# Performance work log

Measured on AMD Instinct MI355X. Metric: run time of the kernel, lower is better.

Reference implementation:

```python
import jax, jax.numpy as jnp
import numpy as np

C = 256
NUM_HEADS = 8
HEAD_DIM = C // NUM_HEADS
SCALE = HEAD_DIM ** -0.5


def setup_inputs() -> dict:
    key = jax.random.key(0)
    ks = jax.random.split(key, 10)
    B, H, W = 2, 64, 64
    s = 0.02
    return {
        "spatial_feat": jax.random.normal(ks[0], (B, C, H, W), jnp.float32),
        "freq_feat": jax.random.normal(ks[1], (B, C, H, W), jnp.float32),
        "wq": jax.random.normal(ks[2], (C, C), jnp.float32) * s,
        "bq": jax.random.normal(ks[3], (C,), jnp.float32) * s,
        "wk": jax.random.normal(ks[4], (C, C), jnp.float32) * s,
        "bk": jax.random.normal(ks[5], (C,), jnp.float32) * s,
        "wv": jax.random.normal(ks[6], (C, C), jnp.float32) * s,
        "bv": jax.random.normal(ks[7], (C,), jnp.float32) * s,
        "wo": jax.random.normal(ks[8], (C, C), jnp.float32) * s,
        "bo": jax.random.normal(ks[9], (C,), jnp.float32) * s,
    }


def _proj(x, w, b):
    # 1x1 conv == channel-mixing matmul: (O,C) x (B,C,H,W) -> (B,O,H,W)
    return jnp.einsum('oc,bchw->bohw', w, x) + b[None, :, None, None]


def _heads(x, B, HW):
    return x.reshape(B, NUM_HEADS, HEAD_DIM, HW)


def _cross_attend(q_src, kv_src, wq, bq, wk, bk, wv, bv, wo, bo):
    B, Cc, H, W = q_src.shape
    HW = H * W
    q = _heads(_proj(q_src, wq, bq), B, HW)   # (B, h, d, N)
    k = _heads(_proj(kv_src, wk, bk), B, HW)
    v = _heads(_proj(kv_src, wv, bv), B, HW)
    # attn[b,h,m,n] = q[...,m] . k[...,n]
    attn = jnp.einsum('bhdm,bhdn->bhmn', q, k) * SCALE
    attn = jax.nn.softmax(attn, axis=-1)
    # out[...,m] = sum_n v[...,n] * attn[m,n]
    out = jnp.einsum('bhdn,bhmn->bhdm', v, attn)
    out = out.reshape(B, Cc, H, W)
    return _proj(out, wo, bo)


def reference(spatial_feat, freq_feat, wq, bq, wk, bk, wv, bv, wo, bo):
    spatial_attended = spatial_feat + _cross_attend(
        spatial_feat, freq_feat, wq, bq, wk, bk, wv, bv, wo, bo)
    freq_attended = freq_feat + _cross_attend(
        freq_feat, spatial_feat, wq, bq, wk, bk, wv, bv, wo, bo)
    return spatial_attended + freq_attended
```

## Files before the change

kernel.cpp:

```cpp
#include <hip/hip_runtime.h>
#include <hip/hip_bf16.h>

#define B_ 2
#define C_ 256
#define NH_ 8
#define D_ 32
#define N_ 4096
#define SCALE_ 0.17677669529663689f
#define QSC_ 0.25505277f

typedef __hip_bfloat16 bf16;
typedef __attribute__((ext_vector_type(8))) short sx8;
typedef __attribute__((ext_vector_type(4))) short sx4;
typedef __attribute__((ext_vector_type(4))) float fx4;
typedef __attribute__((ext_vector_type(4))) int ix4;

__device__ __forceinline__ float b2f(bf16 x) { return __bfloat162float(x); }
__device__ __forceinline__ bf16 f2b(float x) { return __float2bfloat16(x); }
__device__ __forceinline__ short fbs(float x) { bf16 h = __float2bfloat16(x); return *(short*)&h; }
__device__ __forceinline__ float sbf(short s) { bf16 h = *(bf16*)&s; return __bfloat162float(h); }

#if __has_builtin(__builtin_amdgcn_exp2f)
__device__ __forceinline__ float fexp2(float x) { return __builtin_amdgcn_exp2f(x); }
#else
__device__ __forceinline__ float fexp2(float x) { return exp2f(x); }
#endif

__device__ __forceinline__ unsigned pkbf_tr(float x, float y) {
#if __has_builtin(__builtin_amdgcn_perm)
  return __builtin_amdgcn_perm(__builtin_bit_cast(unsigned, y),
                               __builtin_bit_cast(unsigned, x), 0x07060302u);
#else
  unsigned a = __builtin_bit_cast(unsigned, x) >> 16;
  unsigned b = __builtin_bit_cast(unsigned, y) & 0xFFFF0000u;
  return a | b;
#endif
}
__device__ __forceinline__ void pl32swap(unsigned &a, unsigned &b) {
  asm volatile("v_permlane32_swap_b32 %0, %1" : "+v"(a), "+v"(b));
}
__device__ __forceinline__ void pl16swap(unsigned &a, unsigned &b) {
  asm volatile("v_permlane16_swap_b32 %0, %1" : "+v"(a), "+v"(b));
}

__global__ __launch_bounds__(256)
void convert_kernel(const float* __restrict__ spatial,
                    const float* __restrict__ freq,
                    const float* __restrict__ wq, const float* __restrict__ wk,
                    const float* __restrict__ wv, const float* __restrict__ wo,
                    bf16* __restrict__ xb, bf16* __restrict__ wb,
                    bf16* __restrict__ wob) {
  const int tid = threadIdx.x;
  if (blockIdx.z == 4) {
    int base = (blockIdx.y * 64 + blockIdx.x) * 256 + tid;
    #pragma unroll
    for (int i = 0; i < 4; ++i) {
      int idx = base + i * 65536;
      if (idx < 196608) {
        const float* src = (idx < 65536) ? wq : (idx < 131072) ? wk : wv;
        wb[idx] = f2b(src[idx & 65535]);
      } else {
        wob[idx - 196608] = f2b(wo[idx - 196608]);
      }
    }
    return;
  }

  const int p0 = blockIdx.x * 64;
  const int c0 = blockIdx.y * 64;
  const int z  = blockIdx.z;
  const int s = z >> 1, b = z & 1;
  const float* x = (s == 0) ? spatial : freq;

  __shared__ float ls[64][65];

  const int pp = tid & 63, cb = tid >> 6;
  #pragma unroll
  for (int i = 0; i < 16; ++i) {
    int c = cb + 4 * i;
    ls[c][pp] = x[(size_t)(b * C_ + c0 + c) * N_ + p0 + pp];
  }
  __syncthreads();

  #pragma unroll
  for (int i = 0; i < 2; ++i) {
    int j = tid + 256 * i;
    int p = j >> 3, ck = (j & 7) * 8;
    short tmp[8];
    #pragma unroll
    for (int u = 0; u < 8; ++u) tmp[u] = fbs(ls[ck + u][p]);
    *(sx8*)(xb + ((size_t)z * N_ + p0 + p) * C_ + c0 + ck) = *(sx8*)tmp;
  }
}

__global__ __launch_bounds__(256)
void qkv_gemm_kernel(const bf16* __restrict__ wb, const bf16* __restrict__ xb,
                     const float* __restrict__ bq, const float* __restrict__ bk,
                     const float* __restrict__ bv,
                     bf16* __restrict__ qhf, bf16* __restrict__ khf,
                     bf16* __restrict__ vhf) {
  const int tid = threadIdx.x;
  const int p0 = blockIdx.x * 128;
  const int o0 = blockIdx.y * 128;
  const int z  = blockIdx.z;

  const int lane = tid & 63, w = tid >> 6;
  const int ml = lane & 15, Q4 = (lane >> 4) * 4, Q8 = (lane >> 4) * 8;
  const int ow = (w >> 1) * 64, pw = (w & 1) * 64;

  __shared__ __align__(16) short asb[128 * 72];
  __shared__ __align__(16) short bsb[128 * 72];
  __shared__ float bias_s[128];

  if (tid < 128) {
    int o = o0 + tid;
    bias_s[tid] = (o < 256) ? bq[o] : (o < 512) ? bk[o - 256] : bv[o - 512];
  }

  const fx4 z4 = {0.f, 0.f, 0.f, 0.f};
  fx4 acc[4][4];
  #pragma unroll
  for (int ot = 0; ot < 4; ++ot)
    #pragma unroll
    for (int pt = 0; pt < 4; ++pt) acc[ot][pt] = z4;

  const int sr = tid >> 1, scu = (tid & 1) * 32;
  for (int k0 = 0; k0 < 256; k0 += 64) {
    __syncthreads();
    #pragma unroll
    for (int u = 0; u < 4; ++u) {
      *(sx8*)&asb[sr * 72 + scu + u * 8] =
          *(const sx8*)&wb[(o0 + sr) * 256 + k0 + scu + u * 8];
      *(sx8*)&bsb[sr * 72 + scu + u * 8] =
          *(const sx8*)(xb + ((size_t)z * N_ + p0 + sr) * C_ + k0 + scu + u * 8);
    }
    __syncthreads();
    #pragma unroll
    for (int kk = 0; kk < 2; ++kk) {
      sx8 af[4], bfr[4];
      #pragma unroll
      for (int t = 0; t < 4; ++t)
        af[t] = *(sx8*)&asb[(ow + t * 16 + ml) * 72 + kk * 32 + Q8];
      #pragma unroll
      for (int t = 0; t < 4; ++t)
        bfr[t] = *(sx8*)&bsb[(pw + t * 16 + ml) * 72 + kk * 32 + Q8];
      #pragma unroll
      for (int ot = 0; ot < 4; ++ot)
        #pragma unroll
        for (int pt = 0; pt < 4; ++pt)
          acc[ot][pt] = __builtin_amdgcn_mfma_f32_16x16x32_bf16(
              af[ot], bfr[pt], acc[ot][pt], 0, 0, 0);
    }
  }

  if (o0 < 512) {
    bf16* dst = (o0 < 256) ? qhf : khf;
    const int ob = (o0 < 256) ? o0 : o0 - 256;
    const float scl = (o0 < 256) ? QSC_ : 1.f;
    #pragma unroll
    for (int ot = 0; ot < 4; ++ot) {
      const int og = ob + ow + ot * 16 + Q4;
      #pragma unroll
      for (int pt = 0; pt < 4; ++pt) {
        int p = p0 + pw + pt * 16 + ml;
        short tmp[4];
        #pragma unroll
        for (int r = 0; r < 4; ++r)
          tmp[r] = fbs((acc[ot][pt][r] + bias_s[ow + ot * 16 + Q4 + r]) * scl);
        *(sx4*)(dst + (((size_t)z * NH_ + (og >> 5)) * N_ + p) * D_ + (og & 31)) =
            *(sx4*)tmp;
      }
    }
  } else {
    #pragma unroll
    for (int ot = 0; ot < 4; ++ot)
      #pragma unroll
      for (int pt = 0; pt < 4; ++pt) {
        int p = p0 + pw + pt * 16 + ml;
        #pragma unroll
        for (int r = 0; r < 4; ++r) {
          int lo = ow + ot * 16 + Q4 + r;
          int rho = (o0 - 512) + lo;
          int h = rho >> 5, d = rho & 31;
          size_t basev = ((size_t)z * NH_ + h) * D_ * N_;
          vhf[basev + (size_t)(((p >> 5) * 2) + (d >> 4)) * 512 +
              (d & 15) * 32 + (p & 31)] = f2b(acc[ot][pt][r] + bias_s[lo]);
        }
      }
  }
}

__global__ __launch_bounds__(256, 2)
void attn_kernel(const bf16* __restrict__ qhf, const bf16* __restrict__ khf,
                 const bf16* __restrict__ vhf, bf16* __restrict__ attoT) {
  const int tid  = threadIdx.x;
  const int m0   = blockIdx.x * 256;
  const int h    = blockIdx.y;
  const int z    = blockIdx.z;
  const int s = z >> 1, b = z & 1;
  const int zo = ((1 - s) << 1) | b;

  const bf16* qz = qhf + ((size_t)z  * NH_ + h) * N_ * D_;
  const bf16* kz = khf + ((size_t)zo * NH_ + h) * N_ * D_;
  const bf16* vz = vhf + ((size_t)zo * NH_ + h) * D_ * N_;

  const int lane = tid & 63;
  const int w    = tid >> 6;
  const int ml   = lane & 15;
  const int q4   = lane >> 4;
  const int Q4   = q4 * 4;
  const int Q8   = q4 * 8;

  __shared__ __align__(16) short kts[2][64 * 32];
  __shared__ __align__(16) short vss[2][4][16 * 36];

  sx8 qf[4];
  #pragma unroll
  for (int s4 = 0; s4 < 4; ++s4)
    qf[s4] = *(const sx8*)(qz + (size_t)(m0 + w * 64 + s4 * 16 + ml) * D_ + Q8);

  sx8 onesf;
  #pragma unroll
  for (int u = 0; u < 8; ++u) onesf[u] = (short)0x3F80;

  const fx4 z4 = {0.f, 0.f, 0.f, 0.f};
  fx4 acc[4][2];
  #pragma unroll
  for (int s4 = 0; s4 < 4; ++s4) { acc[s4][0] = z4; acc[s4][1] = z4; }
  fx4 lacc[4] = {z4, z4, z4, z4};

  const int srow = tid >> 2;
  const int ksw  = ((tid & 3) ^ (srow & 3)) * 8;
  const int vblk = tid >> 6, vrow = (tid >> 2) & 15, vg = (tid & 3) * 8;
  const int kfg  = (q4 ^ (ml & 3)) * 8;

  sx8 kpre = *(const sx8*)(kz + (size_t)tid * 8);
  sx8 vpre = *(const sx8*)(vz + (size_t)tid * 8);
  *(sx8*)&kts[0][srow * 32 + ksw] = kpre;
  *(sx8*)&vss[0][vblk][vrow * 36 + vg] = vpre;
  __syncthreads();

  int cur = 0;
  for (int n0 = 0; n0 < N_; n0 += 64) {
    const bool more = (n0 + 64 < N_);
    if (more) {
      kpre = *(const sx8*)(kz + (size_t)(n0 + 64) * D_ + (size_t)tid * 8);
      vpre = *(const sx8*)(vz + (size_t)(n0 + 64) * D_ + (size_t)tid * 8);
    }

    sx8 kf[4], vf[2][2];
    #pragma unroll
    for (int t = 0; t < 4; ++t)
      kf[t] = *(sx8*)&kts[cur][(t * 16 + ml) * 32 + kfg];
    #pragma unroll
    for (int dt = 0; dt < 2; ++dt)
      #pragma unroll
      for (int c = 0; c < 2; ++c)
        vf[dt][c] = *(sx8*)&vss[cur][c * 2 + dt][ml * 36 + Q8];

    #pragma unroll
    for (int s4 = 0; s4 < 4; ++s4) {
      fx4 st[4];
      #pragma unroll
      for (int t = 0; t < 4; ++t)
        st[t] = __builtin_amdgcn_mfma_f32_16x16x32_bf16(kf[t], qf[s4], z4, 0, 0, 0);

      unsigned T[4][2];
      #pragma unroll
      for (int t = 0; t < 4; ++t) {
        float e0 = fexp2(st[t][0]), e1 = fexp2(st[t][1]);
        float e2 = fexp2(st[t][2]), e3 = fexp2(st[t][3]);
        T[t][0] = pkbf_tr(e0, e1);
        T[t][1] = pkbf_tr(e2, e3);
      }
      pl32swap(T[0][0], T[1][0]); pl16swap(T[0][0], T[1][0]);
      pl32swap(T[0][1], T[1][1]); pl16swap(T[0][1], T[1][1]);
      pl32swap(T[2][0], T[3][0]); pl16swap(T[2][0], T[3][0]);
      pl32swap(T[2][1], T[3][1]); pl16swap(T[2][1], T[3][1]);
      ix4 p0 = {(int)T[0][0], (int)T[0][1], (int)T[1][0], (int)T[1][1]};
      ix4 p1 = {(int)T[2][0], (int)T[2][1], (int)T[3][0], (int)T[3][1]};
      sx8 pf0 = *(sx8*)&p0;
      sx8 pf1 = *(sx8*)&p1;

      lacc[s4] = __builtin_amdgcn_mfma_f32_16x16x32_bf16(onesf, pf0, lacc[s4], 0, 0, 0);
      lacc[s4] = __builtin_amdgcn_mfma_f32_16x16x32_bf16(onesf, pf1, lacc[s4], 0, 0, 0);
      #pragma unroll
      for (int dt = 0; dt < 2; ++dt) {
        fx4 a = acc[s4][dt];
        a = __builtin_amdgcn_mfma_f32_16x16x32_bf16(vf[dt][0], pf0, a, 0, 0, 0);
        a = __builtin_amdgcn_mfma_f32_16x16x32_bf16(vf[dt][1], pf1, a, 0, 0, 0);
        acc[s4][dt] = a;
      }
    }

    if (more) {
      *(sx8*)&kts[cur ^ 1][srow * 32 + ksw] = kpre;
      *(sx8*)&vss[cur ^ 1][vblk][vrow * 36 + vg] = vpre;
    }
    __syncthreads();
    cur ^= 1;
  }

  #pragma unroll
  for (int s4 = 0; s4 < 4; ++s4) {
    float inv = 1.f / lacc[s4][0];
    int col = m0 + w * 64 + s4 * 16 + ml;
    #pragma unroll
    for (int dt = 0; dt < 2; ++dt) {
      short tmp[4];
      #pragma unroll
      for (int r = 0; r < 4; ++r) tmp[r] = fbs(acc[s4][dt][r] * inv);
      *(sx4*)(attoT + ((size_t)z * N_ + col) * C_ + h * D_ + dt * 16 + Q4) =
          *(sx4*)tmp;
    }
  }
}

__global__ __launch_bounds__(256)
void out_proj_kernel(const bf16* __restrict__ wob, const bf16* __restrict__ attoT,
                     const float* __restrict__ spatial,
                     const float* __restrict__ freq,
                     const float* __restrict__ bo, float* __restrict__ out) {
  const int tid = threadIdx.x;
  const int p0 = blockIdx.x * 64;
  const int o0 = blockIdx.y * 64;
  const int b  = blockIdx.z;

  const int lane = tid & 63, w = tid >> 6;
  const int ml = lane & 15, Q4 = (lane >> 4) * 4, Q8 = (lane >> 4) * 8;
  const int ow = (w >> 1) * 32, pw = (w & 1) * 32;

  __shared__ __align__(16) short asb[64 * 72];
  __shared__ __align__(16) short bsb[64 * 72];
  __shared__ float bo_s[64];

  if (tid < 64) bo_s[tid] = 2.f * bo[o0 + tid];

  const bf16* at0 = attoT + (size_t)(0 + b) * N_ * C_;
  const bf16* at1 = attoT + (size_t)(2 + b) * N_ * C_;

  const fx4 z4 = {0.f, 0.f, 0.f, 0.f};
  fx4 acc[2][2];
  #pragma unroll
  for (int ot = 0; ot < 2; ++ot)
    #pragma unroll
    for (int pt = 0; pt < 2; ++pt) acc[ot][pt] = z4;

  for (int k0 = 0; k0 < 256; k0 += 64) {
    __syncthreads();
    #pragma unroll
    for (int i = 0; i < 2; ++i) {
      int j = tid + 256 * i;
      int r = j >> 3, cu = (j & 7) * 8;
      *(sx8*)&asb[r * 72 + cu] = *(const sx8*)&wob[(o0 + r) * 256 + k0 + cu];
      sx8 va = *(const sx8*)(at0 + (size_t)(p0 + r) * C_ + k0 + cu);
      sx8 vb2 = *(const sx8*)(at1 + (size_t)(p0 + r) * C_ + k0 + cu);
      short tmp[8];
      #pragma unroll
      for (int u = 0; u < 8; ++u) tmp[u] = fbs(sbf(va[u]) + sbf(vb2[u]));
      *(sx8*)&bsb[r * 72 + cu] = *(sx8*)tmp;
    }
    __syncthreads();
    #pragma unroll
    for (int kk = 0; kk < 2; ++kk) {
      sx8 af[2], bfr[2];
      #pragma unroll
      for (int t = 0; t < 2; ++t)
        af[t] = *(sx8*)&asb[(ow + t * 16 + ml) * 72 + kk * 32 + Q8];
      #pragma unroll
      for (int t = 0; t < 2; ++t)
        bfr[t] = *(sx8*)&bsb[(pw + t * 16 + ml) * 72 + kk * 32 + Q8];
      #pragma unroll
      for (int ot = 0; ot < 2; ++ot)
        #pragma unroll
        for (int pt = 0; pt < 2; ++pt)
          acc[ot][pt] = __builtin_amdgcn_mfma_f32_16x16x32_bf16(
              af[ot], bfr[pt], acc[ot][pt], 0, 0, 0);
    }
  }

  #pragma unroll
  for (int ot = 0; ot < 2; ++ot)
    #pragma unroll
    for (int pt = 0; pt < 2; ++pt) {
      int p = p0 + pw + pt * 16 + ml;
      #pragma unroll
      for (int r = 0; r < 4; ++r) {
        int ol = ow + ot * 16 + Q4 + r;
        size_t off = ((size_t)b * C_ + o0 + ol) * N_ + p;
        out[off] = acc[ot][pt][r] + bo_s[ol] + spatial[off] + freq[off];
      }
    }
}

extern "C" void kernel_launch(void* const* d_in, const int* in_sizes, int n_in,
                              void* d_out, int out_size, void* d_ws, size_t ws_size,
                              hipStream_t stream) {
  const float* spatial = (const float*)d_in[0];
  const float* freq    = (const float*)d_in[1];
  const float* wq = (const float*)d_in[2];
  const float* bq = (const float*)d_in[3];
  const float* wk = (const float*)d_in[4];
  const float* bk = (const float*)d_in[5];
  const float* wv = (const float*)d_in[6];
  const float* bv = (const float*)d_in[7];
  const float* wo = (const float*)d_in[8];
  const float* bo = (const float*)d_in[9];
  float* out = (float*)d_out;

  const size_t SZ = (size_t)2 * B_ * N_ * C_;
  bf16* xb    = (bf16*)d_ws;
  bf16* qhf   = xb + SZ;
  bf16* khf   = qhf + SZ;
  bf16* vhf   = khf + SZ;
  bf16* attoT = vhf + SZ;
  bf16* wb    = attoT + SZ;
  bf16* wob   = wb + 768 * 256;

  convert_kernel<<<dim3(N_ / 64, C_ / 64, 5), 256, 0, stream>>>(
      spatial, freq, wq, wk, wv, wo, xb, wb, wob);
  qkv_gemm_kernel<<<dim3(N_ / 128, 768 / 128, 2 * B_), 256, 0, stream>>>(
      wb, xb, bq, bk, bv, qhf, khf, vhf);
  attn_kernel<<<dim3(N_ / 256, NH_, 2 * B_), 256, 0, stream>>>(
      qhf, khf, vhf, attoT);
  out_proj_kernel<<<dim3(N_ / 64, C_ / 64, B_), 256, 0, stream>>>(
      wob, attoT, spatial, freq, bo, out);
}
```

Before: 203.7 us.

## Load K/V fragments directly from global into registers, drop LDS staging

The attention loop no longer stages K and V tiles through double-buffered shared memory with a barrier per tile. Each lane now loads its MFMA fragments straight from global memory into two register sets, prefetching the next tile while computing the current one, and the block-wide syncs are gone. s_setprio is also raised around the MFMA bursts. The aim is to remove LDS traffic and barrier stalls, at the cost of more global/L2 loads, because every wave now fetches the same K/V data, and higher register pressure. On the last iteration the prefetch wraps to tile 0 and loads data that is never used.

```diff
diff --git a/kernel.cpp b/kernel.cpp
--- a/kernel.cpp
+++ b/kernel.cpp
@@ -190,6 +190,50 @@
   }
 }
 
+__device__ __forceinline__ void attn_tile(const sx8 kf[4], const sx8 vf[2][2],
+                                          const sx8 qf[4], sx8 onesf,
+                                          fx4 acc[4][2], fx4 lacc[4]) {
+  const fx4 z4 = {0.f, 0.f, 0.f, 0.f};
+  #pragma unroll
+  for (int s4 = 0; s4 < 4; ++s4) {
+    fx4 st[4];
+    __builtin_amdgcn_s_setprio(1);
+    #pragma unroll
+    for (int t = 0; t < 4; ++t)
+      st[t] = __builtin_amdgcn_mfma_f32_16x16x32_bf16(kf[t], qf[s4], z4, 0, 0, 0);
+    __builtin_amdgcn_s_setprio(0);
+
+    unsigned T[4][2];
+    #pragma unroll
+    for (int t = 0; t < 4; ++t) {
+      float e0 = fexp2(st[t][0]), e1 = fexp2(st[t][1]);
+      float e2 = fexp2(st[t][2]), e3 = fexp2(st[t][3]);
+      T[t][0] = pkbf_tr(e0, e1);
+      T[t][1] = pkbf_tr(e2, e3);
+    }
+    pl32swap(T[0][0], T[1][0]); pl16swap(T[0][0], T[1][0]);
+    pl32swap(T[0][1], T[1][1]); pl16swap(T[0][1], T[1][1]);
+    pl32swap(T[2][0], T[3][0]); pl16swap(T[2][0], T[3][0]);
+    pl32swap(T[2][1], T[3][1]); pl16swap(T[2][1], T[3][1]);
+    ix4 p0 = {(int)T[0][0], (int)T[0][1], (int)T[1][0], (int)T[1][1]};
+    ix4 p1 = {(int)T[2][0], (int)T[2][1], (int)T[3][0], (int)T[3][1]};
+    sx8 pf0 = *(sx8*)&p0;
+    sx8 pf1 = *(sx8*)&p1;
+
+    __builtin_amdgcn_s_setprio(1);
+    lacc[s4] = __builtin_amdgcn_mfma_f32_16x16x32_bf16(onesf, pf0, lacc[s4], 0, 0, 0);
+    lacc[s4] = __builtin_amdgcn_mfma_f32_16x16x32_bf16(onesf, pf1, lacc[s4], 0, 0, 0);
+    #pragma unroll
+    for (int dt = 0; dt < 2; ++dt) {
+      fx4 a = acc[s4][dt];
+      a = __builtin_amdgcn_mfma_f32_16x16x32_bf16(vf[dt][0], pf0, a, 0, 0, 0);
+      a = __builtin_amdgcn_mfma_f32_16x16x32_bf16(vf[dt][1], pf1, a, 0, 0, 0);
+      acc[s4][dt] = a;
+    }
+    __builtin_amdgcn_s_setprio(0);
+  }
+}
+
 __global__ __launch_bounds__(256, 2)
 void attn_kernel(const bf16* __restrict__ qhf, const bf16* __restrict__ khf,
                  const bf16* __restrict__ vhf, bf16* __restrict__ attoT) {
@@ -211,9 +255,6 @@
   const int Q4   = q4 * 4;
   const int Q8   = q4 * 8;
 
-  __shared__ __align__(16) short kts[2][64 * 32];
-  __shared__ __align__(16) short vss[2][4][16 * 36];
-
   sx8 qf[4];
   #pragma unroll
   for (int s4 = 0; s4 < 4; ++s4)
@@ -229,77 +270,40 @@
   for (int s4 = 0; s4 < 4; ++s4) { acc[s4][0] = z4; acc[s4][1] = z4; }
   fx4 lacc[4] = {z4, z4, z4, z4};
 
-  const int srow = tid >> 2;
-  const int ksw  = ((tid & 3) ^ (srow & 3)) * 8;
-  const int vblk = tid >> 6, vrow = (tid >> 2) & 15, vg = (tid & 3) * 8;
-  const int kfg  = (q4 ^ (ml & 3)) * 8;
-
-  sx8 kpre = *(const sx8*)(kz + (size_t)tid * 8);
-  sx8 vpre = *(const sx8*)(vz + (size_t)tid * 8);
-  *(sx8*)&kts[0][srow * 32 + ksw] = kpre;
-  *(sx8*)&vss[0][vblk][vrow * 36 + vg] = vpre;
-  __syncthreads();
-
-  int cur = 0;
-  for (int n0 = 0; n0 < N_; n0 += 64) {
-    const bool more = (n0 + 64 < N_);
-    if (more) {
-      kpre = *(const sx8*)(kz + (size_t)(n0 + 64) * D_ + (size_t)tid * 8);
-      vpre = *(const sx8*)(vz + (size_t)(n0 + 64) * D_ + (size_t)tid * 8);
-    }
-
-    sx8 kf[4], vf[2][2];
-    #pragma unroll
-    for (int t = 0; t < 4; ++t)
-      kf[t] = *(sx8*)&kts[cur][(t * 16 + ml) * 32 + kfg];
-    #pragma unroll
-    for (int dt = 0; dt < 2; ++dt)
-      #pragma unroll
-      for (int c = 0; c < 2; ++c)
-        vf[dt][c] = *(sx8*)&vss[cur][c * 2 + dt][ml * 36 + Q8];
-
-    #pragma unroll
-    for (int s4 = 0; s4 < 4; ++s4) {
-      fx4 st[4];
-      #pragma unroll
-      for (int t = 0; t < 4; ++t)
-        st[t] = __builtin_amdgcn_mfma_f32_16x16x32_bf16(kf[t], qf[s4], z4, 0, 0, 0);
-
-      unsigned T[4][2];
-      #pragma unroll
-      for (int t = 0; t < 4; ++t) {
-        float e0 = fexp2(st[t][0]), e1 = fexp2(st[t][1]);
-        float e2 = fexp2(st[t][2]), e3 = fexp2(st[t][3]);
-        T[t][0] = pkbf_tr(e0, e1);
-        T[t][1] = pkbf_tr(e2, e3);
-      }
-      pl32swap(T[0][0], T[1][0]); pl16swap(T[0][0], T[1][0]);
-      pl32swap(T[0][1], T[1][1]); pl16swap(T[0][1], T[1][1]);
-      pl32swap(T[2][0], T[3][0]); pl16swap(T[2][0], T[3][0]);
-      pl32swap(T[2][1], T[3][1]); pl16swap(T[2][1], T[3][1]);
-      ix4 p0 = {(int)T[0][0], (int)T[0][1], (int)T[1][0], (int)T[1][1]};
-      ix4 p1 = {(int)T[2][0], (int)T[2][1], (int)T[3][0], (int)T[3][1]};
-      sx8 pf0 = *(sx8*)&p0;
-      sx8 pf1 = *(sx8*)&p1;
-
-      lacc[s4] = __builtin_amdgcn_mfma_f32_16x16x32_bf16(onesf, pf0, lacc[s4], 0, 0, 0);
-      lacc[s4] = __builtin_amdgcn_mfma_f32_16x16x32_bf16(onesf, pf1, lacc[s4], 0, 0, 0);
-      #pragma unroll
-      for (int dt = 0; dt < 2; ++dt) {
-        fx4 a = acc[s4][dt];
-        a = __builtin_amdgcn_mfma_f32_16x16x32_bf16(vf[dt][0], pf0, a, 0, 0, 0);
-        a = __builtin_amdgcn_mfma_f32_16x16x32_bf16(vf[dt][1], pf1, a, 0, 0, 0);
-        acc[s4][dt] = a;
-      }
-    }
-
-    if (more) {
-      *(sx8*)&kts[cur ^ 1][srow * 32 + ksw] = kpre;
-      *(sx8*)&vss[cur ^ 1][vblk][vrow * 36 + vg] = vpre;
-    }
-    __syncthreads();
-    cur ^= 1;
-  }
+  const bf16* kbase = kz + (size_t)ml * D_ + Q8;
+  const bf16* vbase = vz + (size_t)ml * 32 + Q8;
+
+#define LDK(n0, kf)                                                          \
+  {                                                                          \
+    _Pragma("unroll") for (int t = 0; t < 4; ++t)                            \
+        kf[t] = *(const sx8*)(kbase + (size_t)((n0) + t * 16) * D_);         \
+  }
+#define LDV(n0, vf)                                                          \
+  {                                                                          \
+    _Pragma("unroll") for (int dt = 0; dt < 2; ++dt)                         \
+        _Pragma("unroll") for (int c = 0; c < 2; ++c)                        \
+            vf[dt][c] = *(const sx8*)(vbase +                                \
+                (size_t)(((n0) >> 5) + c) * 1024 + dt * 512);                \
+  }
+
+  sx8 kfA[4], kfB[4], vfA[2][2], vfB[2][2];
+  LDK(0, kfA);
+  LDV(0, vfA);
+
+  #pragma unroll 1
+  for (int n0 = 0; n0 < N_; n0 += 128) {
+    const int nn = n0 + 64;
+    LDK(nn, kfB);
+    LDV(nn, vfB);
+    attn_tile(kfA, vfA, qf, onesf, acc, lacc);
+
+    const int nn2 = (nn + 64 < N_) ? nn + 64 : 0;
+    LDK(nn2, kfA);
+    LDV(nn2, vfA);
+    attn_tile(kfB, vfB, qf, onesf, acc, lacc);
+  }
+#undef LDK
+#undef LDV
 
   #pragma unroll
   for (int s4 = 0; s4 < 4; ++s4) {
```

Result: faster. 195.1 us (-4.2%).
